# Kernel tuning notes

Hardware: AMD Instinct MI355X
Metric: run time of the kernel (lower is better)

The kernel has to match this reference:

```python
import jax, jax.numpy as jnp
import numpy as np

B, SEQ, NF = 16, 512, 32
E, HID, PRED = 128, 512, 96
N_FFT, HOP, TOPM = 64, 32, 32
W = SEQ // HOP + 1          # 17 windows (centered STFT)
F = N_FFT // 2 + 1          # 33 onesided freqs
LAM = 0.01                  # sparsity_threshold (softshrink)
SCALE = 0.02


def _hann(n):
    # periodic hann, matches torch.hann_window default
    return 0.5 - 0.5 * jnp.cos(2.0 * jnp.pi * jnp.arange(n) / n)


def _softshrink(v):
    return jnp.sign(v) * jnp.maximum(jnp.abs(v) - LAM, 0.0)


def setup_inputs():
    key = jax.random.key(0)
    ks = jax.random.split(key, 12)
    d = {}
    d['x'] = jax.random.normal(ks[0], (B, SEQ, NF), jnp.float32)
    d['embeddings'] = jax.random.normal(ks[1], (1, E), jnp.float32)
    for nm, k in zip(['Wr', 'Wi', 'Wrl', 'Wil', 'Wrr', 'Wir'], ks[2:8]):
        d[nm] = SCALE * jax.random.normal(k, (W, E, E), jnp.float32)
    d['br'] = SCALE * jax.random.normal(ks[8], (W, E), jnp.float32)
    d['bi'] = SCALE * jax.random.normal(ks[9], (W, E), jnp.float32)
    d['fc_w1'] = SCALE * jax.random.normal(ks[10], (SEQ * E, HID), jnp.float32)
    d['fc_b1'] = jnp.zeros((HID,), jnp.float32)
    d['fc_w2'] = SCALE * jax.random.normal(ks[11], (HID, PRED), jnp.float32)
    d['fc_b2'] = jnp.zeros((PRED,), jnp.float32)
    return d


def _forward(x, embeddings, Wr, Wi, Wrl, Wil, Wrr, Wir, br, bi,
             fc_w1, fc_b1, fc_w2, fc_b2):
    Bq, T, N = x.shape
    # tokenEmb: (B,T,N) -> (B,N,T,E)
    xe = x.transpose(0, 2, 1)[..., None] * embeddings
    bias = xe
    # ---- STFT (centered, reflect pad, hann, onesided) ----
    xt = xe.transpose(0, 1, 3, 2)                      # (B,N,E,T)
    pad = N_FFT // 2
    xp = jnp.pad(xt, ((0, 0), (0, 0), (0, 0), (pad, pad)), mode='reflect')
    win = _hann(N_FFT).astype(x.dtype)
    idx = jnp.arange(W)[:, None] * HOP + jnp.arange(N_FFT)[None, :]  # (W,nfft)
    frames = xp[..., idx] * win                        # (B,N,E,W,nfft)
    spec = jnp.fft.rfft(frames, axis=-1)               # (B,N,E,W,F)
    spec = spec.transpose(0, 1, 3, 4, 2)               # (B,N,W,F,E)
    # ---- top-M frequency select (dim=3) ----
    sm = jnp.moveaxis(spec, 3, -1)                     # (B,N,W,E,F)
    _, top_idx = jax.lax.top_k(jnp.abs(sm), TOPM)      # (B,N,W,E,M)
    vals = jnp.take_along_axis(sm, top_idx, axis=-1)
    xw = jnp.moveaxis(vals, -1, 3)                     # (B,N,W,M,E)
    # ---- per-window complex MLP with left/right neighbor windows ----
    z0 = jnp.zeros_like(xw[:, :, :1])
    xl = jnp.concatenate([z0, xw[:, :, :-1]], axis=2)  # left neighbor (zero at w=0)
    xr = jnp.concatenate([xw[:, :, 1:], z0], axis=2)   # right neighbor (zero at w=W-1)

    def cmul(z, wr, wi):
        re = jnp.einsum('bnwme,wef->bnwmf', z.real, wr) - jnp.einsum('bnwme,wef->bnwmf', z.imag, wi)
        im = jnp.einsum('bnwme,wef->bnwmf', z.imag, wr) + jnp.einsum('bnwme,wef->bnwmf', z.real, wi)
        return re, im

    re_m, im_m = cmul(xw, Wr, Wi)
    re_l, im_l = cmul(xl, Wrl, Wil)
    re_r, im_r = cmul(xr, Wrr, Wir)
    o_re = jax.nn.relu(re_m + re_l + re_r + br[None, None, :, None, :])
    o_im = jax.nn.relu(im_m + im_l + im_r + bi[None, None, :, None, :])
    y = _softshrink(o_re) + 1j * _softshrink(o_im)     # (B,N,W,M,E) complex
    # ---- scatter-pad back to full frequency grid ----
    ym = jnp.moveaxis(y, 3, -1)                        # (B,N,W,E,M)
    K = Bq * N * W * E
    flat_vals = ym.reshape(K, TOPM)
    flat_idx = top_idx.reshape(K, TOPM)
    full = jnp.zeros((K, F), ym.dtype).at[jnp.arange(K)[:, None], flat_idx].set(flat_vals)
    spec_full = jnp.moveaxis(full.reshape(Bq, N, W, E, F), -1, 3)  # (B,N,W,F,E)
    # ---- ISTFT (windowed OLA / window-squared envelope, centered trim) ----
    sf = spec_full.transpose(0, 1, 4, 2, 3)            # (B,N,E,W,F)
    fr = jnp.fft.irfft(sf, n=N_FFT, axis=-1) * win     # (B,N,E,W,nfft)
    L = (W - 1) * HOP + N_FFT
    ola = jnp.zeros((Bq, N, E, L), fr.dtype).at[..., idx].add(fr)
    env = jnp.zeros((L,), win.dtype).at[idx].add(win * win)
    ola = ola / jnp.where(env > 1e-11, env, 1.0)
    xt2 = ola[..., pad:L - pad]                        # (B,N,E,T)
    xo = xt2.transpose(0, 1, 3, 2) + bias              # (B,N,T,E) + residual
    # ---- fc head ----
    h = xo.reshape(Bq, N, T * E)
    h = jax.nn.leaky_relu(h @ fc_w1 + fc_b1, 0.01)
    out = h @ fc_w2 + fc_b2                            # (B,N,PRED)
    return out.transpose(0, 2, 1)                      # (B,PRED,N)


def reference(x, embeddings, Wr, Wi, Wrl, Wil, Wrr, Wir, br, bi,
              fc_w1, fc_b1, fc_w2, fc_b2):
    return _forward(x, embeddings, Wr, Wi, Wrl, Wil, Wrr, Wir, br, bi,
                    fc_w1, fc_b1, fc_w2, fc_b2)
```

## Files before the change

kernel.cpp:

```cpp
#include <hip/hip_runtime.h>
#include <hip/hip_bf16.h>

#define LAM 0.01f

typedef __attribute__((ext_vector_type(8))) short v8s;
typedef __attribute__((ext_vector_type(4))) float v4f;

static __device__ __forceinline__ unsigned short f2bf(float f) {
    union { float f; unsigned int u; } v; v.f = f;
    unsigned int u = v.u;
    u += 0x7fffu + ((u >> 16) & 1u);
    return (unsigned short)(u >> 16);
}
static __device__ __forceinline__ float bf2f(unsigned short h) {
    union { unsigned int u; float f; } c; c.u = ((unsigned int)h) << 16;
    return c.f;
}

static __device__ __forceinline__ void async16(const void* g, void* l) {
    __builtin_amdgcn_global_load_lds(
        (const __attribute__((address_space(1))) unsigned int*)g,
        (__attribute__((address_space(3))) unsigned int*)l, 16, 0, 0);
}

#define OFF_COEF 0ull
#define OFF_V    69632ull
#define OFF_BINS 2297856ull
#define OFF_AIMG 3411968ull
#define OFF_W1P  70520832ull
#define OFF_HP   137629696ull

__global__ __launch_bounds__(128) void coef_kernel(
    const float* __restrict__ emb,
    const float* __restrict__ Wr, const float* __restrict__ Wi,
    const float* __restrict__ Wrl, const float* __restrict__ Wil,
    const float* __restrict__ Wrr, const float* __restrict__ Wir,
    const float* __restrict__ br, const float* __restrict__ bi,
    float* __restrict__ coef)
{
    int w = blockIdx.x, j = blockIdx.y, e = threadIdx.x;
    float out;
    if (j < 6) {
        const float* Wj;
        switch (j) {
            case 0: Wj = Wr; break; case 1: Wj = Wi; break;
            case 2: Wj = Wrl; break; case 3: Wj = Wil; break;
            case 4: Wj = Wrr; break; default: Wj = Wir; break;
        }
        const float* p = Wj + (size_t)w * 16384 + e;
        float acc = 0.f;
        #pragma unroll 8
        for (int ep = 0; ep < 128; ++ep) acc = fmaf(emb[ep], p[ep * 128], acc);
        out = acc;
    } else if (j == 6) {
        out = br[w * 128 + e] - LAM;
    } else {
        out = bi[w * 128 + e] - LAM;
    }
    coef[((size_t)(w * 128 + e)) * 8 + j] = out;
}

__global__ __launch_bounds__(256) void stft_kernel(
    const float* __restrict__ x, float2* __restrict__ V, int* __restrict__ bins)
{
    __shared__ float sig[576];
    __shared__ float winT[64];
    __shared__ float2 tw[64];
    __shared__ float2 Sbuf[17 * 33];
    __shared__ float absb[17 * 33];

    const int blk = blockIdx.x;
    const int b = blk >> 5, n = blk & 31;
    const int tid = threadIdx.x;
    const float C64 = 0.09817477042468103f;

    if (tid < 64) {
        float ang = (float)tid * C64;
        winT[tid] = 0.5f - 0.5f * cosf(ang);
        tw[tid] = make_float2(cosf(ang), sinf(ang));
    }
    for (int l = tid; l < 576; l += 256) {
        int t = (l < 32) ? (32 - l) : ((l < 544) ? (l - 32) : (1054 - l));
        sig[l] = x[(size_t)b * 16384 + t * 32 + n];
    }
    __syncthreads();

    for (int task = tid; task < 561; task += 256) {
        int w = task / 33, f = task - w * 33;
        float sr = 0.f, si = 0.f;
        int base = w * 32;
        for (int t = 0; t < 64; ++t) {
            float sw = sig[base + t] * winT[t];
            float2 cs = tw[(f * t) & 63];
            sr = fmaf(sw, cs.x, sr);
            si = fmaf(sw, -cs.y, si);
        }
        Sbuf[task] = make_float2(sr, si);
        absb[task] = sqrtf(fmaf(sr, sr, si * si));
    }
    __syncthreads();

    for (int task = tid; task < 561; task += 256) {
        int w = task / 33, f = task - w * 33;
        float a = absb[task];
        int base = w * 33, rank = 0;
        for (int j = 0; j < 33; ++j) {
            float aj = absb[base + j];
            rank += (aj > a) || (aj == a && j < f);
        }
        if (rank < 32) {
            size_t o = ((size_t)blk * 17 + w) * 32 + rank;
            V[o] = Sbuf[task];
            bins[o] = f;
        }
    }
}

__global__ __launch_bounds__(256) void cvt_kernel(
    const float* __restrict__ w1, unsigned short* __restrict__ w1p)
{
    __shared__ float T[32][132];
    const int kb = blockIdx.x, nt = blockIdx.y;
    const int tid = threadIdx.x;

    #pragma unroll
    for (int p = 0; p < 4; ++p) {
        int r = (tid >> 5) + p * 8;
        int c = (tid & 31) * 4;
        float4 v = *(const float4*)&w1[((size_t)(kb * 32 + r)) * 512 + nt * 128 + c];
        T[r][c] = v.x; T[r][c + 1] = v.y; T[r][c + 2] = v.z; T[r][c + 3] = v.w;
    }
    __syncthreads();

    unsigned short* dst = w1p + ((size_t)nt * 2048 + kb) * 4096;
    #pragma unroll
    for (int p = 0; p < 2; ++p) {
        int pos = tid + 256 * p;
        int np = pos >> 2, cs = pos & 3;
        int clog = cs ^ ((np >> 2) & 3);
        unsigned int pk[4];
        #pragma unroll
        for (int j2 = 0; j2 < 4; ++j2) {
            unsigned short lo = f2bf(T[clog * 8 + j2 * 2][np]);
            unsigned short hi = f2bf(T[clog * 8 + j2 * 2 + 1][np]);
            pk[j2] = (unsigned int)lo | ((unsigned int)hi << 16);
        }
        *(uint4*)&dst[pos * 8] = make_uint4(pk[0], pk[1], pk[2], pk[3]);
    }
}

#define MID_ROLL(J0, J1, J2, J3)                                                \
    {                                                                           \
        _Pragma("unroll") for (int e2 = 0; e2 < 2; ++e2)                        \
        _Pragma("unroll") for (int i = 0; i < 4; ++i) {                         \
            roll[e2][J0][i] = fmaf(acc[0][e2][i], win16[0][i], roll[e2][J0][i]);\
            roll[e2][J1][i] = fmaf(acc[1][e2][i], win16[1][i], roll[e2][J1][i]);\
            roll[e2][J2][i] = fmaf(acc[2][e2][i], win16[2][i], roll[e2][J2][i]);\
            roll[e2][J3][i] = fmaf(acc[3][e2][i], win16[3][i], roll[e2][J3][i]);\
        }                                                                       \
    }

#define MID_FLUSH(JJA, JJB)                                                     \
    {                                                                           \
        _Pragma("unroll") for (int i = 0; i < 4; ++i) {                         \
            int tp = 32 * (w - 1) + q * 4 + i;                                  \
            float xb = xs[tp];                                                  \
            _Pragma("unroll") for (int e2 = 0; e2 < 2; ++e2) {                  \
                float val = fmaf(roll[e2][JJA][i], renv[0][i], xb * emb2[e2]);  \
                Aimg[cbase[e2] + (size_t)tp * 16384] = f2bf(val);               \
                roll[e2][JJA][i] = 0.f;                                         \
            }                                                                   \
            int tp2 = tp + 16;                                                  \
            float xb2 = xs[tp2];                                                \
            _Pragma("unroll") for (int e2 = 0; e2 < 2; ++e2) {                  \
                float val = fmaf(roll[e2][JJB][i], renv[1][i], xb2 * emb2[e2]); \
                Aimg[cbase[e2] + (size_t)tp2 * 16384] = f2bf(val);              \
                roll[e2][JJB][i] = 0.f;                                         \
            }                                                                   \
        }                                                                       \
    }

__global__ __launch_bounds__(256) void mid_kernel(
    const float* __restrict__ x, const float* __restrict__ emb,
    const float* __restrict__ coef, const float2* __restrict__ V,
    const int* __restrict__ bins, unsigned short* __restrict__ Aimg)
{
    __shared__ unsigned short M1t[64 * 72];
    __shared__ unsigned short Yt[128 * 72];
    __shared__ float cosT[64];
    __shared__ float sinT[64];
    __shared__ float2 Vs[17 * 32];
    __shared__ int Bns[17 * 32];
    __shared__ float xs[512];

    const int blk2 = blockIdx.x;
    const int blk = blk2 & 511;
    const int wbeg = (blk2 >> 9) * 8;
    const int b = blk >> 5, n = blk & 31;
    const int tid = threadIdx.x;
    const int wave = tid >> 6, lane = tid & 63, l15 = lane & 15, q = lane >> 4;
    const float C64 = 0.09817477042468103f;

    if (tid < 64) {
        float ang = (float)tid * C64;
        cosT[tid] = __cosf(ang);
        sinT[tid] = __sinf(ang);
    }
    {
        const float2* Vg = V + (size_t)blk * 544;
        const int* Bg = bins + (size_t)blk * 544;
        for (int i = tid; i < 544; i += 256) { Vs[i] = Vg[i]; Bns[i] = Bg[i]; }
        for (int i = tid; i < 512; i += 256) xs[i] = x[(size_t)b * 16384 + i * 32 + n];
    }

    float win16[4][4];
    #pragma unroll
    for (int tt = 0; tt < 4; ++tt)
        #pragma unroll
        for (int i = 0; i < 4; ++i) {
            int t = tt * 16 + q * 4 + i;
            win16[tt][i] = 0.5f - 0.5f * __cosf((float)t * C64);
        }
    float renv[2][4];
    #pragma unroll
    for (int hf = 0; hf < 2; ++hf)
        #pragma unroll
        for (int i = 0; i < 4; ++i) {
            int k = hf * 16 + q * 4 + i;
            float w0 = 0.5f - 0.5f * __cosf((float)k * C64);
            float w1v = 0.5f - 0.5f * __cosf((float)(k + 32) * C64);
            renv[hf][i] = 1.0f / (w0 * w0 + w1v * w1v);
        }
    int ebase[2];
    float emb2[2];
    size_t cbase[2];
    const int mt = blk >> 7, mp = blk & 127, s = (mp >> 2) & 3;
    #pragma unroll
    for (int e2 = 0; e2 < 2; ++e2) {
        ebase[e2] = (wave * 2 + e2) * 16 + l15;
        emb2[e2] = emb[ebase[e2]];
        int e = ebase[e2];
        int echunk = e >> 5, clog = (e >> 3) & 3, cs = clog ^ s, el = e & 7;
        cbase[e2] = ((size_t)mt * 2048 + echunk) * 4096 + mp * 32 + cs * 8 + el;
    }

    float roll[2][4][4];
    #pragma unroll
    for (int e2 = 0; e2 < 2; ++e2)
        #pragma unroll
        for (int jj = 0; jj < 4; ++jj)
            #pragma unroll
            for (int i = 0; i < 4; ++i) roll[e2][jj][i] = 0.f;

    const int e1 = tid & 127;
    const int mg = (tid >> 7) << 4;
    const int tM = tid & 63;
    const int kg = wave << 4;

    __syncthreads();

    for (int w = wbeg; w < wbeg + 9; ++w) {
        {
            const float4* cf = (const float4*)(coef + ((size_t)(w * 128 + e1)) * 8);
            float4 cA = cf[0];
            float4 cB = cf[1];
            unsigned int rep[8], imp[8];
            #pragma unroll
            for (int j2 = 0; j2 < 8; ++j2) {
                unsigned int rpack = 0, ipack = 0;
                #pragma unroll
                for (int sdx = 0; sdx < 2; ++sdx) {
                    int m = mg + j2 * 2 + sdx;
                    float2 vm = Vs[w * 32 + m];
                    float2 vl = (w > 0) ? Vs[(w - 1) * 32 + m] : make_float2(0.f, 0.f);
                    float2 vp = (w < 16) ? Vs[(w + 1) * 32 + m] : make_float2(0.f, 0.f);
                    float re = cB.z;
                    re = fmaf(vm.x, cA.x, re); re = fmaf(-vm.y, cA.y, re);
                    re = fmaf(vl.x, cA.z, re); re = fmaf(-vl.y, cA.w, re);
                    re = fmaf(vp.x, cB.x, re); re = fmaf(-vp.y, cB.y, re);
                    float im = cB.w;
                    im = fmaf(vm.y, cA.x, im); im = fmaf(vm.x, cA.y, im);
                    im = fmaf(vl.y, cA.z, im); im = fmaf(vl.x, cA.w, im);
                    im = fmaf(vp.y, cB.x, im); im = fmaf(vp.x, cB.y, im);
                    re = fmaxf(re, 0.f);
                    im = fmaxf(im, 0.f);
                    rpack |= (unsigned int)f2bf(re) << (16 * sdx);
                    ipack |= (unsigned int)f2bf(im) << (16 * sdx);
                }
                rep[j2] = rpack; imp[j2] = ipack;
            }
            uint4* dr = (uint4*)&Yt[e1 * 72 + mg];
            dr[0] = make_uint4(rep[0], rep[1], rep[2], rep[3]);
            dr[1] = make_uint4(rep[4], rep[5], rep[6], rep[7]);
            uint4* di = (uint4*)&Yt[e1 * 72 + 32 + mg];
            di[0] = make_uint4(imp[0], imp[1], imp[2], imp[3]);
            di[1] = make_uint4(imp[4], imp[5], imp[6], imp[7]);
        }
        {
            unsigned int mpk[8];
            #pragma unroll
            for (int j2 = 0; j2 < 8; ++j2) {
                unsigned int pk = 0;
                #pragma unroll
                for (int sdx = 0; sdx < 2; ++sdx) {
                    int k = kg + j2 * 2 + sdx;
                    int m = k & 31;
                    int r = Bns[w * 32 + m];
                    float sc = (r == 0 || r == 32) ? 0.015625f : 0.03125f;
                    int idx = (r * tM) & 63;
                    float val = (k < 32) ? (cosT[idx] * sc) : (-sinT[idx] * sc);
                    pk |= (unsigned int)f2bf(val) << (16 * sdx);
                }
                mpk[j2] = pk;
            }
            uint4* dm = (uint4*)&M1t[tM * 72 + kg];
            dm[0] = make_uint4(mpk[0], mpk[1], mpk[2], mpk[3]);
            dm[1] = make_uint4(mpk[4], mpk[5], mpk[6], mpk[7]);
        }
        __syncthreads();

        v4f acc[4][2];
        #pragma unroll
        for (int tt = 0; tt < 4; ++tt)
            #pragma unroll
            for (int e2 = 0; e2 < 2; ++e2) acc[tt][e2] = (v4f){0.f, 0.f, 0.f, 0.f};
        #pragma unroll
        for (int ks = 0; ks < 2; ++ks) {
            v8s bfr[2];
            #pragma unroll
            for (int e2 = 0; e2 < 2; ++e2)
                bfr[e2] = *(const v8s*)&Yt[ebase[e2] * 72 + ks * 32 + q * 8];
            #pragma unroll
            for (int tt = 0; tt < 4; ++tt) {
                v8s af = *(const v8s*)&M1t[(tt * 16 + l15) * 72 + ks * 32 + q * 8];
                #pragma unroll
                for (int e2 = 0; e2 < 2; ++e2)
                    acc[tt][e2] = __builtin_amdgcn_mfma_f32_16x16x32_bf16(
                        af, bfr[e2], acc[tt][e2], 0, 0, 0);
            }
        }

        if ((w & 1) == 0) {
            MID_ROLL(0, 1, 2, 3);
            if (w > wbeg) {
                MID_FLUSH(0, 1);
            } else {
                #pragma unroll
                for (int e2 = 0; e2 < 2; ++e2)
                    #pragma unroll
                    for (int i = 0; i < 4; ++i) {
                        roll[e2][0][i] = 0.f; roll[e2][1][i] = 0.f;
                    }
            }
        } else {
            MID_ROLL(2, 3, 0, 1);
            MID_FLUSH(2, 3);
        }
        __syncthreads();
    }
}

__global__ __launch_bounds__(512) void gemm_kernel(
    const unsigned short* __restrict__ Aimg, const unsigned short* __restrict__ w1p,
    unsigned short* __restrict__ hp, int iters, int KS)
{
    __shared__ unsigned short As[2][8192];
    __shared__ unsigned short Bs[2][8192];

    const int gid = blockIdx.x;
    const int xcd = gid & 7;
    const int u = gid >> 3;
    const int KS4 = KS >> 2;
    const int nt2 = (u >= KS4) ? 1 : 0;
    const int vv = u - nt2 * KS4;
    const int pid = vv * 8 + xcd;
    const int ks = pid >> 1;
    const int mt2 = pid & 1;

    const int tid = threadIdx.x;
    const int wave = tid >> 6, lane = tid & 63;
    const int l15 = lane & 15, q = lane >> 4;
    const int kb0 = ks * iters;

    const int isB = wave >> 2;
    const int sub = wave & 3;
    const unsigned short* gsrc = (isB
        ? w1p + ((size_t)(nt2 * 2 + (sub >> 1)) * 2048 + kb0) * 4096
        : Aimg + ((size_t)(mt2 * 2 + (sub >> 1)) * 2048 + kb0) * 4096)
        + (sub & 1) * 2048 + lane * 8;
    const int ldsoff = (sub >> 1) * 4096 + (sub & 1) * 2048;

    v4f acc[4][8];
    #pragma unroll
    for (int mf = 0; mf < 4; ++mf)
        #pragma unroll
        for (int nf = 0; nf < 8; ++nf) acc[mf][nf] = (v4f){0.f, 0.f, 0.f, 0.f};

    {
        unsigned short* dst = (isB ? Bs[0] : As[0]) + ldsoff;
        #pragma unroll
        for (int j = 0; j < 4; ++j) async16(gsrc + j * 512, dst + j * 512);
    }

    const int wm = wave >> 1, wn = wave & 1;
    const int ca = (q ^ ((l15 >> 2) & 3)) * 8;
    const int rA = (wm >> 1) * 4096 + ((wm & 1) * 64 + l15) * 32 + ca;
    const int rB = wn * 4096 + l15 * 32 + ca;

    for (int it = 0; it < iters; ++it) {
        __syncthreads();
        if (it + 1 < iters) {
            const unsigned short* src = gsrc + (size_t)(it + 1) * 4096;
            unsigned short* dst = (isB ? Bs[(it + 1) & 1] : As[(it + 1) & 1]) + ldsoff;
            #pragma unroll
            for (int j = 0; j < 4; ++j) async16(src + j * 512, dst + j * 512);
        }
        const int cur = it & 1;
        v8s af[4], bf[8];
        #pragma unroll
        for (int f = 0; f < 4; ++f) af[f] = *(const v8s*)&As[cur][rA + f * 512];
        #pragma unroll
        for (int nf = 0; nf < 8; ++nf) bf[nf] = *(const v8s*)&Bs[cur][rB + nf * 512];
        #pragma unroll
        for (int mf = 0; mf < 4; ++mf)
            #pragma unroll
            for (int nf = 0; nf < 8; ++nf)
                acc[mf][nf] = __builtin_amdgcn_mfma_f32_16x16x32_bf16(
                    af[mf], bf[nf], acc[mf][nf], 0, 0, 0);
    }

    #pragma unroll
    for (int mf = 0; mf < 4; ++mf)
        #pragma unroll
        for (int nf = 0; nf < 8; ++nf) {
            int row = mt2 * 256 + wm * 64 + mf * 16 + q * 4;
            int col = nt2 * 256 + wn * 128 + nf * 16 + l15;
            unsigned short* dst = hp + ((size_t)ks * 512 + row) * 512 + col;
            #pragma unroll
            for (int i = 0; i < 4; ++i) dst[(size_t)i * 512] = f2bf(acc[mf][nf][i]);
        }
}

__global__ __launch_bounds__(256) void fc2_kernel(
    const unsigned short* __restrict__ hp, const float* __restrict__ b1,
    const float* __restrict__ w2, const float* __restrict__ b2,
    float* __restrict__ out, int KS)
{
    __shared__ float hbuf[512];
    const int row = blockIdx.x;
    const int tid = threadIdx.x;

    const unsigned int* base = (const unsigned int*)(hp + (size_t)row * 512) + tid;
    float a0 = 0.f, a1 = 0.f;
    #pragma unroll 8
    for (int k = 0; k < KS; ++k) {
        unsigned int v = base[(size_t)k * 131072];
        a0 += bf2f((unsigned short)(v & 0xffff));
        a1 += bf2f((unsigned short)(v >> 16));
    }
    float s0 = a0 + b1[tid * 2];
    float s1 = a1 + b1[tid * 2 + 1];
    hbuf[tid * 2]     = (s0 > 0.f) ? s0 : 0.01f * s0;
    hbuf[tid * 2 + 1] = (s1 > 0.f) ? s1 : 0.01f * s1;
    __syncthreads();

    if (tid < 96) {
        float a = b2[tid];
        #pragma unroll 8
        for (int h = 0; h < 512; ++h) a = fmaf(hbuf[h], w2[h * 96 + tid], a);
        int b = row >> 5, n = row & 31;
        out[(size_t)b * 3072 + tid * 32 + n] = a;
    }
}

extern "C" void kernel_launch(void* const* d_in, const int* in_sizes, int n_in,
                              void* d_out, int out_size, void* d_ws, size_t ws_size,
                              hipStream_t stream) {
    const float* x   = (const float*)d_in[0];
    const float* emb = (const float*)d_in[1];
    const float* Wr  = (const float*)d_in[2];
    const float* Wi  = (const float*)d_in[3];
    const float* Wrl = (const float*)d_in[4];
    const float* Wil = (const float*)d_in[5];
    const float* Wrr = (const float*)d_in[6];
    const float* Wir = (const float*)d_in[7];
    const float* br  = (const float*)d_in[8];
    const float* bi  = (const float*)d_in[9];
    const float* w1  = (const float*)d_in[10];
    const float* b1  = (const float*)d_in[11];
    const float* w2  = (const float*)d_in[12];
    const float* b2  = (const float*)d_in[13];

    char* ws = (char*)d_ws;
    float* coef          = (float*)(ws + OFF_COEF);
    float2* V            = (float2*)(ws + OFF_V);
    int* bins            = (int*)(ws + OFF_BINS);
    unsigned short* Aimg = (unsigned short*)(ws + OFF_AIMG);
    unsigned short* w1p  = (unsigned short*)(ws + OFF_W1P);
    unsigned short* hpp  = (unsigned short*)(ws + OFF_HP);

    int KS = 64;
    size_t hp_bytes = (size_t)KS * 512 * 512 * 2;
    if (OFF_HP + hp_bytes > ws_size) {
        KS = 32; hp_bytes = (size_t)KS * 512 * 512 * 2;
    }
    int iters = 2048 / KS;

    coef_kernel<<<dim3(17, 8), dim3(128), 0, stream>>>(
        emb, Wr, Wi, Wrl, Wil, Wrr, Wir, br, bi, coef);
    cvt_kernel<<<dim3(2048, 4), dim3(256), 0, stream>>>(w1, w1p);
    stft_kernel<<<dim3(512), dim3(256), 0, stream>>>(x, V, bins);
    mid_kernel<<<dim3(1024), dim3(256), 0, stream>>>(x, emb, coef, V, bins, Aimg);
    gemm_kernel<<<dim3(4 * KS), dim3(512), 0, stream>>>(Aimg, w1p, hpp, iters, KS);
    fc2_kernel<<<dim3(512), dim3(256), 0, stream>>>(hpp, b1, w2, b2, (float*)d_out, KS);
}
```

Measured before the change: 417.4 us.

## Compute MFMA B-fragments in registers and double-buffer M1t to drop a barrier

The spectral-mixing Y operand is no longer written to shared memory and read back. Each lane now computes the bf16 values it needs for its MFMA B fragment directly in registers, reading V split into separate real and imaginary arrays. M1t is double-buffered by window parity, which lets the trailing per-iteration __syncthreads be removed, and launch bounds request 3 blocks per SM. The changes cut LDS traffic and footprint and one barrier per iteration. In exchange, coefficient loads and FMAs are now repeated per lane, and register pressure rises.

```diff
diff --git a/kernel.cpp b/kernel.cpp
--- a/kernel.cpp
+++ b/kernel.cpp
@@ -180,16 +180,16 @@
         }                                                                       \
     }
 
-__global__ __launch_bounds__(256) void mid_kernel(
+__global__ __launch_bounds__(256, 3) void mid_kernel(
     const float* __restrict__ x, const float* __restrict__ emb,
     const float* __restrict__ coef, const float2* __restrict__ V,
     const int* __restrict__ bins, unsigned short* __restrict__ Aimg)
 {
-    __shared__ unsigned short M1t[64 * 72];
-    __shared__ unsigned short Yt[128 * 72];
+    __shared__ unsigned short M1t[2][64 * 72];
     __shared__ float cosT[64];
     __shared__ float sinT[64];
-    __shared__ float2 Vs[17 * 32];
+    __shared__ __align__(16) float Vre[17 * 32];
+    __shared__ __align__(16) float Vim[17 * 32];
     __shared__ int Bns[17 * 32];
     __shared__ float xs[512];
 
@@ -209,7 +209,11 @@
     {
         const float2* Vg = V + (size_t)blk * 544;
         const int* Bg = bins + (size_t)blk * 544;
-        for (int i = tid; i < 544; i += 256) { Vs[i] = Vg[i]; Bns[i] = Bg[i]; }
+        for (int i = tid; i < 544; i += 256) {
+            float2 v = Vg[i];
+            Vre[i] = v.x; Vim[i] = v.y;
+            Bns[i] = Bg[i];
+        }
         for (int i = tid; i < 512; i += 256) xs[i] = x[(size_t)b * 16384 + i * 32 + n];
     }
 
@@ -252,50 +256,14 @@
             #pragma unroll
             for (int i = 0; i < 4; ++i) roll[e2][jj][i] = 0.f;
 
-    const int e1 = tid & 127;
-    const int mg = (tid >> 7) << 4;
     const int tM = tid & 63;
     const int kg = wave << 4;
+    const float4* coefv = (const float4*)coef;
 
     __syncthreads();
 
     for (int w = wbeg; w < wbeg + 9; ++w) {
-        {
-            const float4* cf = (const float4*)(coef + ((size_t)(w * 128 + e1)) * 8);
-            float4 cA = cf[0];
-            float4 cB = cf[1];
-            unsigned int rep[8], imp[8];
-            #pragma unroll
-            for (int j2 = 0; j2 < 8; ++j2) {
-                unsigned int rpack = 0, ipack = 0;
-                #pragma unroll
-                for (int sdx = 0; sdx < 2; ++sdx) {
-                    int m = mg + j2 * 2 + sdx;
-                    float2 vm = Vs[w * 32 + m];
-                    float2 vl = (w > 0) ? Vs[(w - 1) * 32 + m] : make_float2(0.f, 0.f);
-                    float2 vp = (w < 16) ? Vs[(w + 1) * 32 + m] : make_float2(0.f, 0.f);
-                    float re = cB.z;
-                    re = fmaf(vm.x, cA.x, re); re = fmaf(-vm.y, cA.y, re);
-                    re = fmaf(vl.x, cA.z, re); re = fmaf(-vl.y, cA.w, re);
-                    re = fmaf(vp.x, cB.x, re); re = fmaf(-vp.y, cB.y, re);
-                    float im = cB.w;
-                    im = fmaf(vm.y, cA.x, im); im = fmaf(vm.x, cA.y, im);
-                    im = fmaf(vl.y, cA.z, im); im = fmaf(vl.x, cA.w, im);
-                    im = fmaf(vp.y, cB.x, im); im = fmaf(vp.x, cB.y, im);
-                    re = fmaxf(re, 0.f);
-                    im = fmaxf(im, 0.f);
-                    rpack |= (unsigned int)f2bf(re) << (16 * sdx);
-                    ipack |= (unsigned int)f2bf(im) << (16 * sdx);
-                }
-                rep[j2] = rpack; imp[j2] = ipack;
-            }
-            uint4* dr = (uint4*)&Yt[e1 * 72 + mg];
-            dr[0] = make_uint4(rep[0], rep[1], rep[2], rep[3]);
-            dr[1] = make_uint4(rep[4], rep[5], rep[6], rep[7]);
-            uint4* di = (uint4*)&Yt[e1 * 72 + 32 + mg];
-            di[0] = make_uint4(imp[0], imp[1], imp[2], imp[3]);
-            di[1] = make_uint4(imp[4], imp[5], imp[6], imp[7]);
-        }
+        const int buf = w & 1;
         {
             unsigned int mpk[8];
             #pragma unroll
@@ -313,10 +281,47 @@
                 }
                 mpk[j2] = pk;
             }
-            uint4* dm = (uint4*)&M1t[tM * 72 + kg];
+            uint4* dm = (uint4*)&M1t[buf][tM * 72 + kg];
             dm[0] = make_uint4(mpk[0], mpk[1], mpk[2], mpk[3]);
             dm[1] = make_uint4(mpk[4], mpk[5], mpk[6], mpk[7]);
         }
+
+        unsigned int wre[2][4], wim[2][4];
+        #pragma unroll
+        for (int e2 = 0; e2 < 2; ++e2) {
+            const int e = ebase[e2];
+            float4 cA = coefv[(size_t)(w * 128 + e) * 2];
+            float4 cB = coefv[(size_t)(w * 128 + e) * 2 + 1];
+            #pragma unroll
+            for (int p = 0; p < 4; ++p) {
+                int o = w * 32 + q * 8 + p * 2;
+                float2 vmr = *(const float2*)&Vre[o];
+                float2 vmi = *(const float2*)&Vim[o];
+                float2 vlr = make_float2(0.f, 0.f), vli = vlr;
+                float2 vpr = vlr, vpi = vlr;
+                if (w > 0)  { vlr = *(const float2*)&Vre[o - 32];
+                              vli = *(const float2*)&Vim[o - 32]; }
+                if (w < 16) { vpr = *(const float2*)&Vre[o + 32];
+                              vpi = *(const float2*)&Vim[o + 32]; }
+                float rex = cB.z, rey = cB.z, imx = cB.w, imy = cB.w;
+                rex = fmaf(vmr.x, cA.x, rex);  rey = fmaf(vmr.y, cA.x, rey);
+                rex = fmaf(-vmi.x, cA.y, rex); rey = fmaf(-vmi.y, cA.y, rey);
+                rex = fmaf(vlr.x, cA.z, rex);  rey = fmaf(vlr.y, cA.z, rey);
+                rex = fmaf(-vli.x, cA.w, rex); rey = fmaf(-vli.y, cA.w, rey);
+                rex = fmaf(vpr.x, cB.x, rex);  rey = fmaf(vpr.y, cB.x, rey);
+                rex = fmaf(-vpi.x, cB.y, rex); rey = fmaf(-vpi.y, cB.y, rey);
+                imx = fmaf(vmi.x, cA.x, imx);  imy = fmaf(vmi.y, cA.x, imy);
+                imx = fmaf(vmr.x, cA.y, imx);  imy = fmaf(vmr.y, cA.y, imy);
+                imx = fmaf(vli.x, cA.z, imx);  imy = fmaf(vli.y, cA.z, imy);
+                imx = fmaf(vlr.x, cA.w, imx);  imy = fmaf(vlr.y, cA.w, imy);
+                imx = fmaf(vpi.x, cB.x, imx);  imy = fmaf(vpi.y, cB.x, imy);
+                imx = fmaf(vpr.x, cB.y, imx);  imy = fmaf(vpr.y, cB.y, imy);
+                rex = fmaxf(rex, 0.f); rey = fmaxf(rey, 0.f);
+                imx = fmaxf(imx, 0.f); imy = fmaxf(imy, 0.f);
+                wre[e2][p] = (unsigned int)f2bf(rex) | ((unsigned int)f2bf(rey) << 16);
+                wim[e2][p] = (unsigned int)f2bf(imx) | ((unsigned int)f2bf(imy) << 16);
+            }
+        }
         __syncthreads();
 
         v4f acc[4][2];
@@ -328,11 +333,16 @@
         for (int ks = 0; ks < 2; ++ks) {
             v8s bfr[2];
             #pragma unroll
-            for (int e2 = 0; e2 < 2; ++e2)
-                bfr[e2] = *(const v8s*)&Yt[ebase[e2] * 72 + ks * 32 + q * 8];
+            for (int e2 = 0; e2 < 2; ++e2) {
+                union { uint4 u; v8s v; } cvt;
+                cvt.u = ks == 0
+                    ? make_uint4(wre[e2][0], wre[e2][1], wre[e2][2], wre[e2][3])
+                    : make_uint4(wim[e2][0], wim[e2][1], wim[e2][2], wim[e2][3]);
+                bfr[e2] = cvt.v;
+            }
             #pragma unroll
             for (int tt = 0; tt < 4; ++tt) {
-                v8s af = *(const v8s*)&M1t[(tt * 16 + l15) * 72 + ks * 32 + q * 8];
+                v8s af = *(const v8s*)&M1t[buf][(tt * 16 + l15) * 72 + ks * 32 + q * 8];
                 #pragma unroll
                 for (int e2 = 0; e2 < 2; ++e2)
                     acc[tt][e2] = __builtin_amdgcn_mfma_f32_16x16x32_bf16(
@@ -356,7 +366,6 @@
             MID_ROLL(2, 3, 0, 1);
             MID_FLUSH(2, 3);
         }
-        __syncthreads();
     }
 }
 
```

Measured after the change: 419.5 us. About the same (+0.5%).
